# Kernel tuning notes

Hardware: AMD Instinct MI355X
Metric: run time of the kernel (lower is better)

Reference implementation:

```python
import jax, jax.numpy as jnp
import numpy as np

B, S, H = 4, 2048, 4096   # batch, seq, hidden
Q_DIM = 32 * 128          # num_attention_heads * head_dim
KV_DIM = 8 * 128          # num_key_value_heads * head_dim
R = 16                    # lora_r
SCALING = 32.0 / 16.0     # lora_alpha / lora_r


def setup_inputs() -> dict:
    key = jax.random.key(0)
    ks = jax.random.split(key, 10)
    def n(k, shape, scale):
        return jax.random.normal(k, shape, dtype=jnp.float32) * scale
    x = jax.random.normal(ks[0], (B, S, H), dtype=jnp.float32)
    # base weights stored as [out_dim, in_dim] like nn.Linear
    Wq = n(ks[1], (Q_DIM, H), 0.02)
    Wk = n(ks[2], (KV_DIM, H), 0.02)
    Wv = n(ks[3], (KV_DIM, H), 0.02)
    bq = n(ks[4], (Q_DIM,), 0.02)
    bk = n(ks[5], (KV_DIM,), 0.02)
    bv = n(ks[6], (KV_DIM,), 0.02)
    # LoRA A: kaiming-uniform-like init; B: zeros in training start, use small
    # random values here so the LoRA path is numerically exercised.
    bound = 1.0 / np.sqrt(H)
    Aq = jax.random.uniform(ks[7], (H, R), jnp.float32, -bound, bound)
    Ak = jax.random.uniform(ks[8], (H, R), jnp.float32, -bound, bound)
    Av = jax.random.uniform(ks[9], (H, R), jnp.float32, -bound, bound)
    kb = jax.random.split(jax.random.fold_in(key, 1), 3)
    Bq = n(kb[0], (R, Q_DIM), 0.01)
    Bk = n(kb[1], (R, KV_DIM), 0.01)
    Bv = n(kb[2], (R, KV_DIM), 0.01)
    return {"x": x, "Wq": Wq, "Wk": Wk, "Wv": Wv, "bq": bq, "bk": bk, "bv": bv,
            "Aq": Aq, "Bq": Bq, "Ak": Ak, "Bk": Bk, "Av": Av, "Bv": Bv}


def _proj(x, W, b, A, Bm):
    # base GEMM + low-rank LoRA delta + bias (dropout p=0 -> identity)
    base = jnp.einsum('bsh,oh->bso', x, W)
    delta = jnp.einsum('bsr,ro->bso', jnp.einsum('bsh,hr->bsr', x, A), Bm)
    return base + SCALING * delta + b


def reference(x, Wq, Wk, Wv, bq, bk, bv, Aq, Bq, Ak, Bk, Av, Bv):
    q = _proj(x, Wq, bq, Aq, Bq)  # [B,S,Q_DIM]
    k = _proj(x, Wk, bk, Ak, Bk)  # [B,S,KV_DIM]
    v = _proj(x, Wv, bv, Av, Bv)  # [B,S,KV_DIM]
    return q, k, v
```

## Files before the change

kernel.cpp:

```cpp
#include <hip/hip_runtime.h>


#define GLOBAL_AS __attribute__((address_space(1)))
#define LDS_AS    __attribute__((address_space(3)))

typedef __attribute__((ext_vector_type(8)))  short short8;
typedef __attribute__((ext_vector_type(16))) float f32x16;

constexpr int Mdim = 8192;
constexpr int Kdim = 4096;
constexpr int NQ   = 4096;
constexpr int NKV  = 1024;
constexpr int NTOT = NQ + 2 * NKV;
constexpr float LORA_SCALE = 2.0f;

constexpr int BM = 256, BN = 256;
constexpr int TILES_M = Mdim / BM;
constexpr int TILES_N = NTOT / BN;
constexpr int NWG = TILES_M * TILES_N;
constexpr int NSLICE = Kdim / 32;

constexpr int WEFF_BLOCKS = (NTOT / 64) * (Kdim / 512);
constexpr int CVT_BLOCKS  = 2048;
constexpr int AT_STRIDE   = 516;

__device__ __forceinline__ unsigned short f2bf(float f) {
    union { float f; unsigned int u; } a; a.f = f;
    unsigned int r = a.u + 0x7FFFu + ((a.u >> 16) & 1u);
    return (unsigned short)(r >> 16);
}

__global__ __launch_bounds__(256)
void prep_kernel(const float4* __restrict__ x4, unsigned short* __restrict__ Xbf,
                 const float* __restrict__ Wq, const float* __restrict__ Wk,
                 const float* __restrict__ Wv,
                 const float* __restrict__ Aq, const float* __restrict__ Bq,
                 const float* __restrict__ Ak, const float* __restrict__ Bk,
                 const float* __restrict__ Av, const float* __restrict__ Bv,
                 unsigned short* __restrict__ Wf) {
    __shared__ float AsT[16 * AT_STRIDE];
    __shared__ float Bsc[64 * 16];

    const int tid = threadIdx.x;

    if (blockIdx.x >= WEFF_BLOCKS) {
        int i = (blockIdx.x - WEFF_BLOCKS) * 256 + tid;
        const int stride = CVT_BLOCKS * 256;
        const int n4 = Mdim * Kdim / 4;
        ushort4* out = (ushort4*)Xbf;
        for (; i < n4; i += stride) {
            float4 v = x4[i];
            ushort4 u;
            u.x = f2bf(v.x); u.y = f2bf(v.y); u.z = f2bf(v.z); u.w = f2bf(v.w);
            out[i] = u;
        }
        return;
    }

    const int n0 = (blockIdx.x >> 3) * 64;
    const int h0 = (blockIdx.x & 7) * 512;

    const float* W; const float* A; const float* Bm; int O; int nn0;
    if (n0 < NQ)            { W = Wq; A = Aq; Bm = Bq; O = NQ;  nn0 = n0; }
    else if (n0 < NQ + NKV) { W = Wk; A = Ak; Bm = Bk; O = NKV; nn0 = n0 - NQ; }
    else                    { W = Wv; A = Av; Bm = Bv; O = NKV; nn0 = n0 - NQ - NKV; }

    {
        const float4* Af4 = (const float4*)(A) + h0 * 4;
        #pragma unroll
        for (int i = 0; i < 8; ++i) {
            const int f = i * 256 + tid;
            const float4 v = Af4[f];
            const int hl = f >> 2;
            const int r0 = (f & 3) * 4;
            AsT[(r0 + 0) * AT_STRIDE + hl] = v.x;
            AsT[(r0 + 1) * AT_STRIDE + hl] = v.y;
            AsT[(r0 + 2) * AT_STRIDE + hl] = v.z;
            AsT[(r0 + 3) * AT_STRIDE + hl] = v.w;
        }
    }
    {
        const int nl = tid & 63;
        const int rq = tid >> 6;
        #pragma unroll
        for (int j = 0; j < 4; ++j) {
            const int r = rq * 4 + j;
            Bsc[nl * 16 + r] = Bm[r * O + nn0 + nl] * LORA_SCALE;
        }
    }
    __syncthreads();

    const int wv_ = tid >> 6;
    const int lane = tid & 63;

    #pragma unroll
    for (int pass = 0; pass < 2; ++pass) {
        const int hl = pass * 256 + lane * 4;
        float4 areg[16];
        #pragma unroll
        for (int r = 0; r < 16; ++r)
            areg[r] = *(const float4*)(&AsT[r * AT_STRIDE + hl]);

        for (int i = 0; i < 16; ++i) {
            const int nl = wv_ * 16 + i;
            const float4 w4 = *(const float4*)(W + (size_t)(nn0 + nl) * Kdim + h0 + hl);
            const float4* b4 = (const float4*)(&Bsc[nl * 16]);
            float4 d = {0.f, 0.f, 0.f, 0.f};
            #pragma unroll
            for (int q = 0; q < 4; ++q) {
                const float4 b = b4[q];
                d.x += areg[q*4+0].x * b.x + areg[q*4+1].x * b.y + areg[q*4+2].x * b.z + areg[q*4+3].x * b.w;
                d.y += areg[q*4+0].y * b.x + areg[q*4+1].y * b.y + areg[q*4+2].y * b.z + areg[q*4+3].y * b.w;
                d.z += areg[q*4+0].z * b.x + areg[q*4+1].z * b.y + areg[q*4+2].z * b.z + areg[q*4+3].z * b.w;
                d.w += areg[q*4+0].w * b.x + areg[q*4+1].w * b.y + areg[q*4+2].w * b.z + areg[q*4+3].w * b.w;
            }
            ushort4 u;
            u.x = f2bf(w4.x + d.x); u.y = f2bf(w4.y + d.y);
            u.z = f2bf(w4.z + d.z); u.w = f2bf(w4.w + d.w);
            *(ushort4*)(Wf + (size_t)(n0 + nl) * Kdim + h0 + hl) = u;
        }
    }
}

__global__ __launch_bounds__(512, 2)
void gemm_qkv_kernel(const unsigned short* __restrict__ X,
                     const unsigned short* __restrict__ Wf,
                     const float* __restrict__ bq, const float* __restrict__ bk,
                     const float* __restrict__ bv,
                     float* __restrict__ out) {
    __shared__ __align__(16) unsigned short Abuf[4][8192];
    __shared__ __align__(16) unsigned short Bbuf[4][8192];

    const int tid  = threadIdx.x;
    const int lane = tid & 63;
    const int w    = tid >> 6;
    const int wr   = w >> 2;
    const int wc   = w & 3;

    int bid = blockIdx.x;
    bid = (bid & 7) * (NWG / 8) + (bid >> 3);
    const int row0 = (bid / TILES_N) * BM;
    const int col0 = (bid % TILES_N) * BN;

    const int aRow0 = (wr * 128 + (lane & 31)) * 64;
    const int bRow0 = (wc * 64  + (lane & 31)) * 64;
    int ckswz[2];
    #pragma unroll
    for (int ks = 0; ks < 2; ++ks)
        ckswz[ks] = (((ks * 2 + (lane >> 5)) ^ ((lane >> 1) & 3)) << 4);

    const int srow = (w << 4) + (lane >> 2);
    const int kswz = (((lane & 3) ^ ((lane >> 3) & 3)) << 3);
    const unsigned short* pA0 = X  + (size_t)(row0 + srow) * Kdim + kswz;
    const unsigned short* pA1 = pA0 + (size_t)128 * Kdim;
    const unsigned short* pB0 = Wf + (size_t)(col0 + srow) * Kdim + kswz;
    const unsigned short* pB1 = pB0 + (size_t)128 * Kdim;

    f32x16 acc[4][2];
    #pragma unroll
    for (int i = 0; i < 4; ++i)
        #pragma unroll
        for (int j = 0; j < 2; ++j)
            acc[i][j] = (f32x16)(0.f);

    short8 bfr[2][2];

#define STAGE(MATA, SS)                                                          \
    { const int ss_ = (SS); const int st_ = (SS) & 3;                            \
      if (MATA) {                                                                \
        __builtin_amdgcn_global_load_lds((const GLOBAL_AS void*)(pA0 + ss_ * 32),\
            (LDS_AS void*)(&Abuf[st_][w * 512]),        16, 0, 0);               \
        __builtin_amdgcn_global_load_lds((const GLOBAL_AS void*)(pA1 + ss_ * 32),\
            (LDS_AS void*)(&Abuf[st_][4096 + w * 512]), 16, 0, 0);               \
      } else {                                                                   \
        __builtin_amdgcn_global_load_lds((const GLOBAL_AS void*)(pB0 + ss_ * 32),\
            (LDS_AS void*)(&Bbuf[st_][w * 512]),        16, 0, 0);               \
        __builtin_amdgcn_global_load_lds((const GLOBAL_AS void*)(pB1 + ss_ * 32),\
            (LDS_AS void*)(&Bbuf[st_][4096 + w * 512]), 16, 0, 0);               \
      } }

#define DO_PHASE(G, MH, DOSTAGE, SMATA, SS, WAITMODE)                            \
    {                                                                            \
      const int slot_ = (G) & 3;                                                 \
      const char* abase_ = (const char*)Abuf + slot_ * 16384;                    \
      short8 af[2][2];                                                           \
      _Pragma("unroll")                                                          \
      for (int m = 0; m < 2; ++m)                                                \
        _Pragma("unroll")                                                        \
        for (int ks = 0; ks < 2; ++ks)                                           \
          af[m][ks] = *(const short8*)(abase_ + aRow0 + (MH) * 4096 + m * 2048   \
                                       + ckswz[ks]);                             \
      if ((MH) == 0) {                                                           \
        const char* bbase_ = (const char*)Bbuf + slot_ * 16384;                  \
        _Pragma("unroll")                                                        \
        for (int n = 0; n < 2; ++n)                                              \
          _Pragma("unroll")                                                      \
          for (int ks = 0; ks < 2; ++ks)                                         \
            bfr[n][ks] = *(const short8*)(bbase_ + bRow0 + n * 2048 + ckswz[ks]);\
      }                                                                          \
      if (DOSTAGE) STAGE(SMATA, SS);                                             \
      __builtin_amdgcn_s_barrier();                                              \
      asm volatile("s_waitcnt lgkmcnt(0)");                                      \
      __builtin_amdgcn_s_setprio(1);                                             \
      _Pragma("unroll")                                                          \
      for (int ks = 0; ks < 2; ++ks)                                             \
        _Pragma("unroll")                                                        \
        for (int m = 0; m < 2; ++m)                                              \
          _Pragma("unroll")                                                      \
          for (int n = 0; n < 2; ++n)                                            \
            acc[(MH) * 2 + m][n] = __builtin_amdgcn_mfma_f32_32x32x16_bf16(      \
                af[m][ks], bfr[n][ks], acc[(MH) * 2 + m][n], 0, 0, 0);           \
      __builtin_amdgcn_s_setprio(0);                                             \
      if ((WAITMODE) == 1) asm volatile("s_waitcnt vmcnt(4)" ::: "memory");      \
      if ((WAITMODE) == 2) asm volatile("s_waitcnt vmcnt(0)" ::: "memory");      \
      __builtin_amdgcn_s_barrier();                                              \
    }

    STAGE(1, 0); STAGE(0, 0);
    STAGE(1, 1); STAGE(0, 1);
    STAGE(1, 2); STAGE(0, 2);
    asm volatile("s_waitcnt vmcnt(4)" ::: "memory");
    __builtin_amdgcn_s_barrier();

    for (int j = 0; j < NSLICE / 4 - 1; ++j) {
        const int g0 = j * 4;
        DO_PHASE(g0 + 0, 0, 1, 1, g0 + 3, 0);
        DO_PHASE(g0 + 0, 1, 1, 0, g0 + 3, 0);
        DO_PHASE(g0 + 1, 0, 1, 1, g0 + 4, 0);
        DO_PHASE(g0 + 1, 1, 1, 0, g0 + 4, 1);
        DO_PHASE(g0 + 2, 0, 1, 1, g0 + 5, 0);
        DO_PHASE(g0 + 2, 1, 1, 0, g0 + 5, 0);
        DO_PHASE(g0 + 3, 0, 1, 1, g0 + 6, 0);
        DO_PHASE(g0 + 3, 1, 1, 0, g0 + 6, 1);
    }
    DO_PHASE(124, 0, 1, 1, 127, 0);
    DO_PHASE(124, 1, 1, 0, 127, 0);
    DO_PHASE(125, 0, 0, 0, 0,   0);
    DO_PHASE(125, 1, 0, 0, 0,   1);
    DO_PHASE(126, 0, 0, 0, 0,   0);
    DO_PHASE(126, 1, 0, 0, 0,   2);
    DO_PHASE(127, 0, 0, 0, 0,   0);
    DO_PHASE(127, 1, 0, 0, 0,   0);

#undef DO_PHASE
#undef STAGE

    float* obase; int ldo; const float* bias; int cofs;
    if (col0 < NQ) {
        obase = out;                             ldo = NQ;  bias = bq; cofs = 0;
    } else if (col0 < NQ + NKV) {
        obase = out + (size_t)Mdim * NQ;         ldo = NKV; bias = bk; cofs = NQ;
    } else {
        obase = out + (size_t)Mdim * (NQ + NKV); ldo = NKV; bias = bv; cofs = NQ + NKV;
    }

    #pragma unroll
    for (int nf2 = 0; nf2 < 2; ++nf2) {
        const int col = col0 + wc * 64 + nf2 * 32 + (lane & 31) - cofs;
        const float b = bias[col];
        #pragma unroll
        for (int mf2 = 0; mf2 < 4; ++mf2) {
            #pragma unroll
            for (int r = 0; r < 16; ++r) {
                const int row = row0 + wr * 128 + mf2 * 32
                              + ((lane >> 5) << 2) + (r & 3) + ((r >> 2) << 3);
                obase[(size_t)row * ldo + col] = acc[mf2][nf2][r] + b;
            }
        }
    }
}

extern "C" void kernel_launch(void* const* d_in, const int* in_sizes, int n_in,
                              void* d_out, int out_size, void* d_ws, size_t ws_size,
                              hipStream_t stream) {
    const float* x  = (const float*)d_in[0];
    const float* Wq = (const float*)d_in[1];
    const float* Wk = (const float*)d_in[2];
    const float* Wv = (const float*)d_in[3];
    const float* bq = (const float*)d_in[4];
    const float* bk = (const float*)d_in[5];
    const float* bv = (const float*)d_in[6];
    const float* Aq = (const float*)d_in[7];
    const float* Bq = (const float*)d_in[8];
    const float* Ak = (const float*)d_in[9];
    const float* Bk = (const float*)d_in[10];
    const float* Av = (const float*)d_in[11];
    const float* Bv = (const float*)d_in[12];
    float* out = (float*)d_out;

    unsigned short* Xbf = (unsigned short*)d_ws;
    unsigned short* Wf  = Xbf + (size_t)Mdim * Kdim;

    prep_kernel<<<WEFF_BLOCKS + CVT_BLOCKS, 256, 0, stream>>>(
        (const float4*)x, Xbf, Wq, Wk, Wv, Aq, Bq, Ak, Bk, Av, Bv, Wf);

    gemm_qkv_kernel<<<NWG, 512, 0, stream>>>(Xbf, Wf, bq, bk, bv, out);
}
```

Baseline: 482.8 us.

## Pre-swizzle bf16 operands in global memory and read LDS fragments as 8-byte halves

The fp32-to-bf16 conversion of x and the fused-weight kernel now write their outputs with an XOR swizzle of 8-byte groups keyed on the row index. The GEMM's global-to-LDS loads therefore use plain contiguous offsets. Each 16-byte fragment read from LDS becomes two 8-byte reads at swizzled positions. The aim is to reduce LDS bank conflicts with a finer-grained swizzle than the old 16-byte scheme. The cost is twice as many LDS read instructions and output tensors that only this GEMM's swizzle convention can consume.

```diff
diff --git a/kernel.cpp b/kernel.cpp
--- a/kernel.cpp
+++ b/kernel.cpp
@@ -5,6 +5,7 @@
 #define LDS_AS    __attribute__((address_space(3)))
 
 typedef __attribute__((ext_vector_type(8)))  short short8;
+typedef __attribute__((ext_vector_type(4)))  short short4v;
 typedef __attribute__((ext_vector_type(16))) float f32x16;
 
 constexpr int Mdim = 8192;
@@ -52,7 +53,9 @@
             float4 v = x4[i];
             ushort4 u;
             u.x = f2bf(v.x); u.y = f2bf(v.y); u.z = f2bf(v.z); u.w = f2bf(v.w);
-            out[i] = u;
+            const int r = i >> 10;
+            const int key = (r >> 1) & 7;
+            out[(i & ~7) | ((i & 7) ^ key)] = u;
         }
         return;
     }
@@ -117,7 +120,10 @@
             ushort4 u;
             u.x = f2bf(w4.x + d.x); u.y = f2bf(w4.y + d.y);
             u.z = f2bf(w4.z + d.z); u.w = f2bf(w4.w + d.w);
-            *(ushort4*)(Wf + (size_t)(n0 + nl) * Kdim + h0 + hl) = u;
+            const int n = n0 + nl;
+            const int key = (n >> 1) & 7;
+            const int hs = (h0 + hl & ~31) | ((((h0 + hl) >> 2 & 7) ^ key) << 2);
+            *(ushort4*)(Wf + (size_t)n * Kdim + hs) = u;
         }
     }
 }
@@ -144,16 +150,20 @@
 
     const int aRow0 = (wr * 128 + (lane & 31)) * 64;
     const int bRow0 = (wc * 64  + (lane & 31)) * 64;
-    int ckswz[2];
+    const int key   = (lane >> 1) & 7;
+    int gofs[2][2];
     #pragma unroll
-    for (int ks = 0; ks < 2; ++ks)
-        ckswz[ks] = (((ks * 2 + (lane >> 5)) ^ ((lane >> 1) & 3)) << 4);
+    for (int ks = 0; ks < 2; ++ks) {
+        const int g = ks * 4 + (lane >> 5) * 2;
+        gofs[ks][0] = ((g    ) ^ key) << 3;
+        gofs[ks][1] = ((g + 1) ^ key) << 3;
+    }
 
     const int srow = (w << 4) + (lane >> 2);
-    const int kswz = (((lane & 3) ^ ((lane >> 3) & 3)) << 3);
-    const unsigned short* pA0 = X  + (size_t)(row0 + srow) * Kdim + kswz;
+    const int kofs = (lane & 3) * 8;
+    const unsigned short* pA0 = X  + (size_t)(row0 + srow) * Kdim + kofs;
     const unsigned short* pA1 = pA0 + (size_t)128 * Kdim;
-    const unsigned short* pB0 = Wf + (size_t)(col0 + srow) * Kdim + kswz;
+    const unsigned short* pB0 = Wf + (size_t)(col0 + srow) * Kdim + kofs;
     const unsigned short* pB1 = pB0 + (size_t)128 * Kdim;
 
     f32x16 acc[4][2];
@@ -164,6 +174,11 @@
             acc[i][j] = (f32x16)(0.f);
 
     short8 bfr[2][2];
+
+#define LDFRAG(DST, BASE, ROWB, KS)                                              \
+    { short4v lo_ = *(const short4v*)((BASE) + (ROWB) + gofs[KS][0]);            \
+      short4v hi_ = *(const short4v*)((BASE) + (ROWB) + gofs[KS][1]);            \
+      DST = __builtin_shufflevector(lo_, hi_, 0, 1, 2, 3, 4, 5, 6, 7); }
 
 #define STAGE(MATA, SS)                                                          \
     { const int ss_ = (SS); const int st_ = (SS) & 3;                            \
@@ -188,15 +203,14 @@
       for (int m = 0; m < 2; ++m)                                                \
         _Pragma("unroll")                                                        \
         for (int ks = 0; ks < 2; ++ks)                                           \
-          af[m][ks] = *(const short8*)(abase_ + aRow0 + (MH) * 4096 + m * 2048   \
-                                       + ckswz[ks]);                             \
+          LDFRAG(af[m][ks], abase_, aRow0 + (MH) * 4096 + m * 2048, ks);         \
       if ((MH) == 0) {                                                           \
         const char* bbase_ = (const char*)Bbuf + slot_ * 16384;                  \
         _Pragma("unroll")                                                        \
         for (int n = 0; n < 2; ++n)                                              \
           _Pragma("unroll")                                                      \
           for (int ks = 0; ks < 2; ++ks)                                         \
-            bfr[n][ks] = *(const short8*)(bbase_ + bRow0 + n * 2048 + ckswz[ks]);\
+            LDFRAG(bfr[n][ks], bbase_, bRow0 + n * 2048, ks);                    \
       }                                                                          \
       if (DOSTAGE) STAGE(SMATA, SS);                                             \
       __builtin_amdgcn_s_barrier();                                              \
@@ -244,6 +258,7 @@
 
 #undef DO_PHASE
 #undef STAGE
+#undef LDFRAG
 
     float* obase; int ldo; const float* bias; int cofs;
     if (col0 < NQ) {
```

After: 518.0 us. +7.3%, slower.

## Use fragment-ordered LDS layout for staging and add nontemporal output stores

Applied to the files above, without the earlier changes.

Changes how each wave stages A/B tiles into LDS so that every lane writes and reads its MFMA fragment contiguously. Each lane now loads 16 bytes of one row at two k offsets, and fragment reads become lane*16 plus constant offsets, with no XOR swizzle. This removes the swizzle address math and aims to avoid LDS bank conflicts. The epilogue also switches to nontemporal stores for the large fp32 output, to avoid polluting the cache. The risk is that the new global access pattern, with 32 rows per wave and 64-byte pieces per row, may coalesce less well.

```diff
diff --git a/kernel.cpp b/kernel.cpp
--- a/kernel.cpp
+++ b/kernel.cpp
@@ -142,19 +142,14 @@
     const int row0 = (bid / TILES_N) * BM;
     const int col0 = (bid % TILES_N) * BN;
 
-    const int aRow0 = (wr * 128 + (lane & 31)) * 64;
-    const int bRow0 = (wc * 64  + (lane & 31)) * 64;
-    int ckswz[2];
-    #pragma unroll
-    for (int ks = 0; ks < 2; ++ks)
-        ckswz[ks] = (((ks * 2 + (lane >> 5)) ^ ((lane >> 1) & 3)) << 4);
-
-    const int srow = (w << 4) + (lane >> 2);
-    const int kswz = (((lane & 3) ^ ((lane >> 3) & 3)) << 3);
-    const unsigned short* pA0 = X  + (size_t)(row0 + srow) * Kdim + kswz;
-    const unsigned short* pA1 = pA0 + (size_t)128 * Kdim;
-    const unsigned short* pB0 = Wf + (size_t)(col0 + srow) * Kdim + kswz;
-    const unsigned short* pB1 = pB0 + (size_t)128 * Kdim;
+    const int lane16 = lane * 16;
+    const int aBase0 = wr * 8192 + lane16;
+    const int bBase0 = wc * 4096 + lane16;
+
+    const int srow = w * 32 + (lane & 31);
+    const int kofs = (lane >> 5) * 8;
+    const unsigned short* pA = X  + (size_t)(row0 + srow) * Kdim + kofs;
+    const unsigned short* pB = Wf + (size_t)(col0 + srow) * Kdim + kofs;
 
     f32x16 acc[4][2];
     #pragma unroll
@@ -168,15 +163,15 @@
 #define STAGE(MATA, SS)                                                          \
     { const int ss_ = (SS); const int st_ = (SS) & 3;                            \
       if (MATA) {                                                                \
-        __builtin_amdgcn_global_load_lds((const GLOBAL_AS void*)(pA0 + ss_ * 32),\
-            (LDS_AS void*)(&Abuf[st_][w * 512]),        16, 0, 0);               \
-        __builtin_amdgcn_global_load_lds((const GLOBAL_AS void*)(pA1 + ss_ * 32),\
-            (LDS_AS void*)(&Abuf[st_][4096 + w * 512]), 16, 0, 0);               \
+        __builtin_amdgcn_global_load_lds((const GLOBAL_AS void*)(pA + ss_ * 32), \
+            (LDS_AS void*)(&Abuf[st_][(w * 2 + 0) * 512]), 16, 0, 0);            \
+        __builtin_amdgcn_global_load_lds((const GLOBAL_AS void*)(pA + ss_ * 32 + 16), \
+            (LDS_AS void*)(&Abuf[st_][(w * 2 + 1) * 512]), 16, 0, 0);            \
       } else {                                                                   \
-        __builtin_amdgcn_global_load_lds((const GLOBAL_AS void*)(pB0 + ss_ * 32),\
-            (LDS_AS void*)(&Bbuf[st_][w * 512]),        16, 0, 0);               \
-        __builtin_amdgcn_global_load_lds((const GLOBAL_AS void*)(pB1 + ss_ * 32),\
-            (LDS_AS void*)(&Bbuf[st_][4096 + w * 512]), 16, 0, 0);               \
+        __builtin_amdgcn_global_load_lds((const GLOBAL_AS void*)(pB + ss_ * 32), \
+            (LDS_AS void*)(&Bbuf[st_][(w * 2 + 0) * 512]), 16, 0, 0);            \
+        __builtin_amdgcn_global_load_lds((const GLOBAL_AS void*)(pB + ss_ * 32 + 16), \
+            (LDS_AS void*)(&Bbuf[st_][(w * 2 + 1) * 512]), 16, 0, 0);            \
       } }
 
 #define DO_PHASE(G, MH, DOSTAGE, SMATA, SS, WAITMODE)                            \
@@ -188,15 +183,15 @@
       for (int m = 0; m < 2; ++m)                                                \
         _Pragma("unroll")                                                        \
         for (int ks = 0; ks < 2; ++ks)                                           \
-          af[m][ks] = *(const short8*)(abase_ + aRow0 + (MH) * 4096 + m * 2048   \
-                                       + ckswz[ks]);                             \
+          af[m][ks] = *(const short8*)(abase_ + aBase0 +                         \
+                          (((MH) * 2 + m) * 2 + ks) * 1024);                     \
       if ((MH) == 0) {                                                           \
         const char* bbase_ = (const char*)Bbuf + slot_ * 16384;                  \
         _Pragma("unroll")                                                        \
         for (int n = 0; n < 2; ++n)                                              \
           _Pragma("unroll")                                                      \
           for (int ks = 0; ks < 2; ++ks)                                         \
-            bfr[n][ks] = *(const short8*)(bbase_ + bRow0 + n * 2048 + ckswz[ks]);\
+            bfr[n][ks] = *(const short8*)(bbase_ + bBase0 + (n * 2 + ks) * 1024);\
       }                                                                          \
       if (DOSTAGE) STAGE(SMATA, SS);                                             \
       __builtin_amdgcn_s_barrier();                                              \
@@ -255,16 +250,17 @@
     }
 
     #pragma unroll
-    for (int nf2 = 0; nf2 < 2; ++nf2) {
-        const int col = col0 + wc * 64 + nf2 * 32 + (lane & 31) - cofs;
+    for (int nf = 0; nf < 2; ++nf) {
+        const int col = col0 + wc * 64 + nf * 32 + (lane & 31) - cofs;
         const float b = bias[col];
         #pragma unroll
-        for (int mf2 = 0; mf2 < 4; ++mf2) {
+        for (int mf = 0; mf < 4; ++mf) {
             #pragma unroll
             for (int r = 0; r < 16; ++r) {
-                const int row = row0 + wr * 128 + mf2 * 32
+                const int row = row0 + wr * 128 + mf * 32
                               + ((lane >> 5) << 2) + (r & 3) + ((r >> 2) << 3);
-                obase[(size_t)row * ldo + col] = acc[mf2][nf2][r] + b;
+                __builtin_nontemporal_store(acc[mf][nf][r] + b,
+                                            &obase[(size_t)row * ldo + col]);
             }
         }
     }
```

Result: slower. 552.4 us (+14.4%).
